# Performance work log

Hardware: AMD Instinct MI355X
Metric: run time of the kernel (lower is better)

The kernel has to match this reference:

```python
import jax, jax.numpy as jnp
import numpy as np

N_NODES = 100000
N_EDGES = 1600000
IN_DIM = 64
EMBED_DIM = 128
OUT_DIM = 10


def setup_inputs() -> dict:
    key = jax.random.key(0)
    ks = jax.random.split(key, 12)
    x = jax.random.normal(ks[0], (N_NODES, IN_DIM), dtype=jnp.float32)
    edge_index = jax.random.randint(ks[1], (2, N_EDGES), 0, N_NODES, dtype=jnp.int64)
    s = lambda k, shp, fan_in: jax.random.normal(k, shp, dtype=jnp.float32) / np.sqrt(fan_in)
    # SAGEConv params: lin_l (applied to aggregated neighbors, has bias), lin_r (root, no bias)
    W_l = s(ks[2], (IN_DIM, EMBED_DIM), IN_DIM)
    b_l = jnp.zeros((EMBED_DIM,), dtype=jnp.float32)
    W_r = s(ks[3], (IN_DIM, EMBED_DIM), IN_DIM)
    # Classifier MLP: embed -> 64 -> 128 -> out
    W1 = s(ks[4], (EMBED_DIM, 64), EMBED_DIM)
    b1 = jnp.zeros((64,), dtype=jnp.float32)
    W2 = s(ks[5], (64, 128), 64)
    b2 = jnp.zeros((128,), dtype=jnp.float32)
    W3 = s(ks[6], (128, OUT_DIM), 128)
    b3 = jnp.zeros((OUT_DIM,), dtype=jnp.float32)
    return {"x": x, "edge_index": edge_index, "W_l": W_l, "b_l": b_l, "W_r": W_r,
            "W1": W1, "b1": b1, "W2": W2, "b2": b2, "W3": W3, "b3": b3}


def reference(x, edge_index, W_l, b_l, W_r, W1, b1, W2, b2, W3, b3):
    src, dst = edge_index[0], edge_index[1]
    # mean-aggregate neighbor features: gather x[src], scatter-sum to dst, divide by degree
    msg = x[src]                                                   # [E, in_dim]
    agg = jax.ops.segment_sum(msg, dst, num_segments=N_NODES)      # [N, in_dim]
    deg = jax.ops.segment_sum(jnp.ones((src.shape[0],), x.dtype), dst, num_segments=N_NODES)
    mean = agg / jnp.maximum(deg, 1.0)[:, None]                    # [N, in_dim]
    # SAGEConv: lin_l(mean_neigh) + lin_r(x_root)
    h = mean @ W_l + b_l + x @ W_r                                 # [N, embed_dim]
    # classifier MLP (logits)
    h = jax.nn.relu(h @ W1 + b1)
    h = jax.nn.relu(h @ W2 + b2)
    return h @ W3 + b3
```

## Files before the change

### kernel.cpp

```cpp
#include <hip/hip_runtime.h>
#include <hip/hip_bf16.h>

#define N_NODES 100000
#define IN_DIM 64
#define EMB 128
#define HID1 64
#define HID2 128
#define OUT_DIM 10

#define CHUNK 4096
#define EPT   (CHUNK / 256)
#define NBUCK ((N_NODES + 511) >> 9)
#define CAPB 9216

#define NB_CONV ((N_NODES * 16) / 256)
#define WCAT_N (128 * 128)
#define W1T_N  (64 * 128)
#define W2T_N  (128 * 64)
#define W3T_N  (16 * 128)
#define PREP_TOT (WCAT_N + W1T_N + W2T_N + W3T_N)
#define NB_PREP ((PREP_TOT + 255) / 256)

using short8 = __attribute__((ext_vector_type(8))) short;
using bfx4   = __attribute__((ext_vector_type(4))) short;
using f32x4  = __attribute__((ext_vector_type(4))) float;

__device__ inline short f2bf(float f) {
  __hip_bfloat16 h = __float2bfloat16(f);
  return *reinterpret_cast<short*>(&h);
}

struct BinShared {
  int hist[NBUCK], excl[NBUCK], cur[NBUCK], gb[NBUCK];
  int stage[CHUNK];
  unsigned char bof[CHUNK];
  int sc[256];
};

__global__ __launch_bounds__(256) void frontend_kernel(
    const float* __restrict__ x,
    const int* __restrict__ src, const int* __restrict__ dst,
    const float* __restrict__ W_l, const float* __restrict__ W_r,
    const float* __restrict__ W1, const float* __restrict__ W2,
    const float* __restrict__ W3,
    int* __restrict__ gcur, int* __restrict__ ebuf, short* __restrict__ comb,
    short* __restrict__ wcat_t, short* __restrict__ w1t,
    short* __restrict__ w2t, short* __restrict__ w3t,
    int E, int nbC)
{
  __shared__ __align__(16) char smem_raw[sizeof(BinShared)];
  const int b = blockIdx.x;
  const int tid = threadIdx.x;

  if (b < nbC) {
    BinShared& S = *reinterpret_cast<BinShared*>(smem_raw);
    const int base = b * CHUNK;
    const int cn = min(CHUNK, E - base);

    int dreg[EPT];
#pragma unroll
    for (int it = 0; it < EPT; ++it) {
      int i = tid + it * 256;
      dreg[it] = (i < cn) ? dst[base + i] : -1;
    }

    for (int i = tid; i < NBUCK; i += 256) S.hist[i] = 0;
    __syncthreads();
#pragma unroll
    for (int it = 0; it < EPT; ++it)
      if (dreg[it] >= 0) atomicAdd(&S.hist[dreg[it] >> 9], 1);
    __syncthreads();

    int v = (tid < NBUCK) ? S.hist[tid] : 0;
    S.sc[tid] = v;
    __syncthreads();
    for (int off = 1; off < 256; off <<= 1) {
      int u = (tid >= off) ? S.sc[tid - off] : 0;
      __syncthreads();
      S.sc[tid] += u;
      __syncthreads();
    }
    if (tid < NBUCK) {
      int ex = S.sc[tid] - v;
      S.excl[tid] = ex; S.cur[tid] = ex;
      S.gb[tid] = v ? atomicAdd(&gcur[tid], v) : 0;
    }
    __syncthreads();

#pragma unroll
    for (int it = 0; it < EPT; ++it) {
      int i = tid + it * 256;
      if (i < cn) {
        int d = dreg[it], s = src[base + i];
        int bk = d >> 9;
        int pos = atomicAdd(&S.cur[bk], 1);
        S.stage[pos] = ((d & 511) << 17) | s;
        S.bof[pos] = (unsigned char)bk;
      }
    }
    __syncthreads();

    for (int i = tid; i < cn; i += 256) {
      int bk = S.bof[i];
      int idx = S.gb[bk] + (i - S.excl[bk]);
      if (idx < CAPB) ebuf[bk * CAPB + idx] = S.stage[i];
    }
  } else if (b < nbC + NB_CONV) {
    int t = (b - nbC) * 256 + tid;
    int node = t >> 4, g = t & 15;
    f32x4 v = *(const f32x4*)&x[(size_t)node * IN_DIM + g * 4];
    bfx4 s;
#pragma unroll
    for (int i = 0; i < 4; ++i) s[i] = f2bf(v[i]);
    *(bfx4*)&comb[((size_t)node << 7) + g * 4] = s;
  } else {
    int t = (b - nbC - NB_CONV) * 256 + tid;
    if (t < WCAT_N) {
      int c = t >> 7, k = t & 127;
      float v = (k < 64) ? W_r[k * EMB + c] : W_l[(k - 64) * EMB + c];
      wcat_t[c * 128 + k] = f2bf(v);
    } else if (t < WCAT_N + W1T_N) {
      int u = t - WCAT_N;
      int c = u >> 7, k = u & 127;
      w1t[c * 128 + k] = f2bf(W1[k * HID1 + c]);
    } else if (t < WCAT_N + W1T_N + W2T_N) {
      int u = t - WCAT_N - W1T_N;
      int c = u >> 6, k = u & 63;
      w2t[c * 64 + k] = f2bf(W2[k * HID2 + c]);
    } else if (t < PREP_TOT) {
      int u = t - WCAT_N - W1T_N - W2T_N;
      int c = u >> 7, k = u & 127;
      w3t[c * 128 + k] = (c < OUT_DIM) ? f2bf(W3[k * OUT_DIM + c]) : (short)0;
    }
  }
}

__global__ __launch_bounds__(256) void bucket_csr(
    const int* __restrict__ gcur, int* __restrict__ ebuf,
    int* __restrict__ offs, int* __restrict__ oend)
{
  __shared__ int cnt[512], cur[512], sc[512];
  __shared__ int ep[CAPB];
  __shared__ int es[CAPB];
  const int b = blockIdx.x, tid = threadIdx.x;
  const int node0 = b << 9;
  const int nn = min(512, N_NODES - node0);
  const int ebase = b * CAPB;
  const int ecnt = min(gcur[b], CAPB);

  for (int i = tid; i < 512; i += 256) cnt[i] = 0;
  __syncthreads();
  for (int i = tid; i < ecnt; i += 256) {
    int p = ebuf[ebase + i];
    ep[i] = p;
    atomicAdd(&cnt[p >> 17], 1);
  }
  __syncthreads();
  for (int i = tid; i < 512; i += 256) sc[i] = cnt[i];
  __syncthreads();
  for (int off = 1; off < 512; off <<= 1) {
    int i0 = tid, i1 = tid + 256;
    int v0 = (i0 >= off) ? sc[i0 - off] : 0;
    int v1 = (i1 >= off) ? sc[i1 - off] : 0;
    __syncthreads();
    sc[i0] += v0; sc[i1] += v1;
    __syncthreads();
  }
  for (int i = tid; i < 512; i += 256) {
    int ex = sc[i] - cnt[i];
    cur[i] = ex;
    if (i < nn) {
      offs[node0 + i] = ebase + ex;
      oend[node0 + i] = ebase + sc[i];
    }
  }
  __syncthreads();
  for (int i = tid; i < ecnt; i += 256) {
    int p = ep[i];
    int pos = atomicAdd(&cur[p >> 17], 1);
    es[pos] = p & 131071;
  }
  __syncthreads();
  for (int i = tid; i < ecnt; i += 256) ebuf[ebase + i] = es[i];
}

__global__ __launch_bounds__(256) void aggregate_kernel(
    const int* __restrict__ offs, const int* __restrict__ oend,
    const int* __restrict__ esrc, short* __restrict__ comb)
{
  int wv = (int)((blockIdx.x * 256 + threadIdx.x) >> 6);
  const int lane = threadIdx.x & 63;
  const int node = __builtin_amdgcn_readfirstlane(wv);
  if (node >= N_NODES) return;
  const int beg = offs[node];
  const int end = oend[node];
  const int deg = end - beg;
  const unsigned short* cb = (const unsigned short*)comb;
  float a = 0.f;

  int k = beg;
  for (; k + 16 <= end; k += 16) {
    unsigned o0  = ((unsigned)esrc[k]      << 7) + lane;
    unsigned o1  = ((unsigned)esrc[k + 1]  << 7) + lane;
    unsigned o2  = ((unsigned)esrc[k + 2]  << 7) + lane;
    unsigned o3  = ((unsigned)esrc[k + 3]  << 7) + lane;
    unsigned o4  = ((unsigned)esrc[k + 4]  << 7) + lane;
    unsigned o5  = ((unsigned)esrc[k + 5]  << 7) + lane;
    unsigned o6  = ((unsigned)esrc[k + 6]  << 7) + lane;
    unsigned o7  = ((unsigned)esrc[k + 7]  << 7) + lane;
    unsigned o8  = ((unsigned)esrc[k + 8]  << 7) + lane;
    unsigned o9  = ((unsigned)esrc[k + 9]  << 7) + lane;
    unsigned o10 = ((unsigned)esrc[k + 10] << 7) + lane;
    unsigned o11 = ((unsigned)esrc[k + 11] << 7) + lane;
    unsigned o12 = ((unsigned)esrc[k + 12] << 7) + lane;
    unsigned o13 = ((unsigned)esrc[k + 13] << 7) + lane;
    unsigned o14 = ((unsigned)esrc[k + 14] << 7) + lane;
    unsigned o15 = ((unsigned)esrc[k + 15] << 7) + lane;
    unsigned u0  = cb[o0],  u1  = cb[o1],  u2  = cb[o2],  u3  = cb[o3];
    unsigned u4  = cb[o4],  u5  = cb[o5],  u6  = cb[o6],  u7  = cb[o7];
    unsigned u8  = cb[o8],  u9  = cb[o9],  u10 = cb[o10], u11 = cb[o11];
    unsigned u12 = cb[o12], u13 = cb[o13], u14 = cb[o14], u15 = cb[o15];
    a += __uint_as_float(u0  << 16); a += __uint_as_float(u1  << 16);
    a += __uint_as_float(u2  << 16); a += __uint_as_float(u3  << 16);
    a += __uint_as_float(u4  << 16); a += __uint_as_float(u5  << 16);
    a += __uint_as_float(u6  << 16); a += __uint_as_float(u7  << 16);
    a += __uint_as_float(u8  << 16); a += __uint_as_float(u9  << 16);
    a += __uint_as_float(u10 << 16); a += __uint_as_float(u11 << 16);
    a += __uint_as_float(u12 << 16); a += __uint_as_float(u13 << 16);
    a += __uint_as_float(u14 << 16); a += __uint_as_float(u15 << 16);
  }
  if (k + 8 <= end) {
    unsigned o0 = ((unsigned)esrc[k]     << 7) + lane;
    unsigned o1 = ((unsigned)esrc[k + 1] << 7) + lane;
    unsigned o2 = ((unsigned)esrc[k + 2] << 7) + lane;
    unsigned o3 = ((unsigned)esrc[k + 3] << 7) + lane;
    unsigned o4 = ((unsigned)esrc[k + 4] << 7) + lane;
    unsigned o5 = ((unsigned)esrc[k + 5] << 7) + lane;
    unsigned o6 = ((unsigned)esrc[k + 6] << 7) + lane;
    unsigned o7 = ((unsigned)esrc[k + 7] << 7) + lane;
    unsigned u0 = cb[o0], u1 = cb[o1], u2 = cb[o2], u3 = cb[o3];
    unsigned u4 = cb[o4], u5 = cb[o5], u6 = cb[o6], u7 = cb[o7];
    a += __uint_as_float(u0 << 16); a += __uint_as_float(u1 << 16);
    a += __uint_as_float(u2 << 16); a += __uint_as_float(u3 << 16);
    a += __uint_as_float(u4 << 16); a += __uint_as_float(u5 << 16);
    a += __uint_as_float(u6 << 16); a += __uint_as_float(u7 << 16);
    k += 8;
  }
  if (k + 4 <= end) {
    unsigned o0 = ((unsigned)esrc[k]     << 7) + lane;
    unsigned o1 = ((unsigned)esrc[k + 1] << 7) + lane;
    unsigned o2 = ((unsigned)esrc[k + 2] << 7) + lane;
    unsigned o3 = ((unsigned)esrc[k + 3] << 7) + lane;
    unsigned u0 = cb[o0], u1 = cb[o1], u2 = cb[o2], u3 = cb[o3];
    a += __uint_as_float(u0 << 16); a += __uint_as_float(u1 << 16);
    a += __uint_as_float(u2 << 16); a += __uint_as_float(u3 << 16);
    k += 4;
  }
  for (; k < end; ++k) {
    unsigned u0 = cb[((unsigned)esrc[k] << 7) + lane];
    a += __uint_as_float(u0 << 16);
  }

  float m = a / fmaxf((float)deg, 1.0f);
  ((unsigned short*)comb)[((size_t)node << 7) + 64 + lane] =
      (unsigned short)f2bf(m);
}

#define PA 128
#define PH 64

__global__ __launch_bounds__(256) void fused_mfma_kernel(
    const short* __restrict__ comb,
    const short* __restrict__ wcat_t, const short* __restrict__ w1t,
    const short* __restrict__ w2t, const short* __restrict__ w3t,
    const float* __restrict__ b_l, const float* __restrict__ b1,
    const float* __restrict__ b2, const float* __restrict__ b3,
    float* __restrict__ out)
{
  __shared__ __align__(16) short sA0[64 * PA];
  __shared__ __align__(16) short sH [64 * PA];
  __shared__ __align__(16) short sH1[64 * PH];
  __shared__ __align__(16) short sW [128 * PA];

  const int tid  = threadIdx.x;
  const int base = blockIdx.x * 64;
  const int lane = tid & 63;
  const int w    = tid >> 6;
  const int lrow = lane & 15;
  const int lgrp = lane >> 4;

  for (int T = tid; T < 1024; T += 256) {
    int n = T >> 4, g = T & 15;
    int node = base + n;
    short8 s = {0, 0, 0, 0, 0, 0, 0, 0};
    if (node < N_NODES) s = *(const short8*)&comb[(size_t)node * 128 + 8 * g];
    *(short8*)&sA0[(n * PA + 8 * g) ^ ((n & 7) << 3)] = s;
  }
  for (int T = tid; T < 2048; T += 256) {
    int c = T >> 4, kg = T & 15;
    *(short8*)&sW[(c * PA + 8 * kg) ^ ((c & 7) << 3)] =
        *(const short8*)&wcat_t[c * 128 + 8 * kg];
  }
  __syncthreads();

  {
    const int c0w = 32 * w;
    short8 bf[2][4];
#pragma unroll
    for (int ct = 0; ct < 2; ++ct)
#pragma unroll
      for (int kk = 0; kk < 4; ++kk) {
        int row = c0w + 16 * ct + lrow;
        bf[ct][kk] = *(const short8*)&sW[(row * PA + kk * 32 + lgrp * 8) ^ ((row & 7) << 3)];
      }
#pragma unroll
    for (int rt = 0; rt < 4; ++rt) {
      short8 af[4];
#pragma unroll
      for (int kk = 0; kk < 4; ++kk) {
        int row = rt * 16 + lrow;
        af[kk] = *(const short8*)&sA0[(row * PA + kk * 32 + lgrp * 8) ^ ((row & 7) << 3)];
      }
#pragma unroll
      for (int ct = 0; ct < 2; ++ct) {
        float bv = b_l[c0w + 16 * ct + lrow];
        f32x4 acc = {bv, bv, bv, bv};
#pragma unroll
        for (int kk = 0; kk < 4; ++kk)
          acc = __builtin_amdgcn_mfma_f32_16x16x32_bf16(af[kk], bf[ct][kk], acc, 0, 0, 0);
        int col = c0w + 16 * ct + lrow;
        int rb = rt * 16 + lgrp * 4;
#pragma unroll
        for (int r = 0; r < 4; ++r) {
          int row = rb + r;
          sH[(row * PA + col) ^ ((row & 7) << 3)] = f2bf(acc[r]);
        }
      }
    }
  }
  __syncthreads();

  for (int T = tid; T < 1024; T += 256) {
    int c = T >> 4, kg = T & 15;
    *(short8*)&sW[(c * PA + 8 * kg) ^ ((c & 7) << 3)] =
        *(const short8*)&w1t[c * 128 + 8 * kg];
  }
  {
    int c = tid >> 4, kg = tid & 15;
    *(short8*)&sA0[(c * PA + 8 * kg) ^ ((c & 7) << 3)] =
        *(const short8*)&w3t[c * 128 + 8 * kg];
  }
  __syncthreads();

  {
    const int c0 = 16 * w;
    short8 bf[4];
#pragma unroll
    for (int kk = 0; kk < 4; ++kk) {
      int row = c0 + lrow;
      bf[kk] = *(const short8*)&sW[(row * PA + kk * 32 + lgrp * 8) ^ ((row & 7) << 3)];
    }
#pragma unroll
    for (int rt = 0; rt < 4; ++rt) {
      short8 af[4];
#pragma unroll
      for (int kk = 0; kk < 4; ++kk) {
        int row = rt * 16 + lrow;
        af[kk] = *(const short8*)&sH[(row * PA + kk * 32 + lgrp * 8) ^ ((row & 7) << 3)];
      }
      float bv = b1[c0 + lrow];
      f32x4 acc = {bv, bv, bv, bv};
#pragma unroll
      for (int kk = 0; kk < 4; ++kk)
        acc = __builtin_amdgcn_mfma_f32_16x16x32_bf16(af[kk], bf[kk], acc, 0, 0, 0);
      int col = c0 + lrow;
      int rb = rt * 16 + lgrp * 4;
#pragma unroll
      for (int r = 0; r < 4; ++r) {
        int row = rb + r;
        sH1[(row * PH + col) ^ ((row & 7) << 3)] = f2bf(fmaxf(acc[r], 0.f));
      }
    }
  }
  __syncthreads();

  for (int T = tid; T < 1024; T += 256) {
    int c = T >> 3, kg = T & 7;
    *(short8*)&sW[(c * PA + 8 * kg) ^ ((c & 7) << 3)] =
        *(const short8*)&w2t[c * 64 + 8 * kg];
  }
  __syncthreads();

  {
    const int c0w = 32 * w;
    short8 bf[2][2];
#pragma unroll
    for (int ct = 0; ct < 2; ++ct)
#pragma unroll
      for (int kk = 0; kk < 2; ++kk) {
        int row = c0w + 16 * ct + lrow;
        bf[ct][kk] = *(const short8*)&sW[(row * PA + kk * 32 + lgrp * 8) ^ ((row & 7) << 3)];
      }
#pragma unroll
    for (int rt = 0; rt < 4; ++rt) {
      short8 af[2];
#pragma unroll
      for (int kk = 0; kk < 2; ++kk) {
        int row = rt * 16 + lrow;
        af[kk] = *(const short8*)&sH1[(row * PH + kk * 32 + lgrp * 8) ^ ((row & 7) << 3)];
      }
#pragma unroll
      for (int ct = 0; ct < 2; ++ct) {
        float bv = b2[c0w + 16 * ct + lrow];
        f32x4 acc = {bv, bv, bv, bv};
#pragma unroll
        for (int kk = 0; kk < 2; ++kk)
          acc = __builtin_amdgcn_mfma_f32_16x16x32_bf16(af[kk], bf[ct][kk], acc, 0, 0, 0);
        int col = c0w + 16 * ct + lrow;
        int rb = rt * 16 + lgrp * 4;
#pragma unroll
        for (int r = 0; r < 4; ++r) {
          int row = rb + r;
          sH[(row * PA + col) ^ ((row & 7) << 3)] = f2bf(fmaxf(acc[r], 0.f));
        }
      }
    }
  }
  __syncthreads();

  {
    short8 af[4], bf[4];
#pragma unroll
    for (int kk = 0; kk < 4; ++kk) {
      int row = 16 * w + lrow;
      af[kk] = *(const short8*)&sH[(row * PA + kk * 32 + lgrp * 8) ^ ((row & 7) << 3)];
      bf[kk] = *(const short8*)&sA0[(lrow * PA + kk * 32 + lgrp * 8) ^ ((lrow & 7) << 3)];
    }
    float bv = (lrow < OUT_DIM) ? b3[lrow] : 0.f;
    f32x4 acc = {bv, bv, bv, bv};
#pragma unroll
    for (int kk = 0; kk < 4; ++kk)
      acc = __builtin_amdgcn_mfma_f32_16x16x32_bf16(af[kk], bf[kk], acc, 0, 0, 0);
#pragma unroll
    for (int r = 0; r < 4; ++r) {
      int row = 16 * w + lgrp * 4 + r;
      int node = base + row;
      if (node < N_NODES && lrow < OUT_DIM)
        out[(long long)node * OUT_DIM + lrow] = acc[r];
    }
  }
}

extern "C" void kernel_launch(void* const* d_in, const int* in_sizes, int n_in,
                              void* d_out, int out_size, void* d_ws, size_t ws_size,
                              hipStream_t stream) {
  const float* x   = (const float*)d_in[0];
  const int*   ei  = (const int*)d_in[1];
  const float* W_l = (const float*)d_in[2];
  const float* b_l = (const float*)d_in[3];
  const float* W_r = (const float*)d_in[4];
  const float* W1  = (const float*)d_in[5];
  const float* b1  = (const float*)d_in[6];
  const float* W2  = (const float*)d_in[7];
  const float* b2  = (const float*)d_in[8];
  const float* W3  = (const float*)d_in[9];
  const float* b3  = (const float*)d_in[10];
  float* out = (float*)d_out;

  const int E = in_sizes[1] / 2;
  const int* src = ei;
  const int* dst = ei + E;

  short* wcat_t = (short*)d_ws;
  short* w1t    = wcat_t + WCAT_N;
  short* w2t    = w1t + W1T_N;
  short* w3t    = w2t + W2T_N;
  short* comb   = w3t + W3T_N;
  int*   offs   = (int*)(comb + (size_t)N_NODES * 128);
  int*   oend   = offs + N_NODES;
  int*   ebuf   = oend + N_NODES;
  int*   gcur   = ebuf + (size_t)NBUCK * CAPB;

  (void)hipMemsetAsync(gcur, 0, NBUCK * sizeof(int), stream);

  const int nbC = (E + CHUNK - 1) / CHUNK;
  frontend_kernel<<<nbC + NB_CONV + NB_PREP, 256, 0, stream>>>(
      x, src, dst, W_l, W_r, W1, W2, W3,
      gcur, ebuf, comb, wcat_t, w1t, w2t, w3t, E, nbC);

  bucket_csr<<<NBUCK, 256, 0, stream>>>(gcur, ebuf, offs, oend);

  int nbAgg = (N_NODES * 64 + 255) / 256;
  aggregate_kernel<<<nbAgg, 256, 0, stream>>>(offs, oend, ebuf, comb);

  int nbF = (N_NODES + 63) / 64;
  fused_mfma_kernel<<<nbF, 256, 0, stream>>>(comb, wcat_t, w1t, w2t, w3t,
                                             b_l, b1, b2, b3, out);
}
```

Before: 109.5 us.

## Double fused MLP tile to 128 nodes with 512-thread blocks

The fused MFMA kernel now handles 128 nodes per block with 8 waves instead of 64 nodes with 4 waves. The work split is rearranged so each wave owns one 16-column slice across all rows, and the second layer splits rows across two wave groups. This amortises the per-block staging of weights into LDS over more nodes, but raises LDS use per block, which may limit how many blocks fit on a CU and how well barriers overlap. The binning shared arrays are also padded to 256 entries so the scan write-back loses its thread guard.

```diff
diff --git a/kernel.cpp b/kernel.cpp
--- a/kernel.cpp
+++ b/kernel.cpp
@@ -31,7 +31,7 @@
 }
 
 struct BinShared {
-  int hist[NBUCK], excl[NBUCK], cur[NBUCK], gb[NBUCK];
+  int hist[256], excl[256], cur[256], gb[256];
   int stage[CHUNK];
   unsigned char bof[CHUNK];
   int sc[256];
@@ -64,7 +64,7 @@
       dreg[it] = (i < cn) ? dst[base + i] : -1;
     }
 
-    for (int i = tid; i < NBUCK; i += 256) S.hist[i] = 0;
+    for (int i = tid; i < 256; i += 256) S.hist[i] = 0;
     __syncthreads();
 #pragma unroll
     for (int it = 0; it < EPT; ++it)
@@ -80,10 +80,10 @@
       S.sc[tid] += u;
       __syncthreads();
     }
-    if (tid < NBUCK) {
+    {
       int ex = S.sc[tid] - v;
       S.excl[tid] = ex; S.cur[tid] = ex;
-      S.gb[tid] = v ? atomicAdd(&gcur[tid], v) : 0;
+      S.gb[tid] = (tid < NBUCK && v) ? atomicAdd(&gcur[tid], v) : 0;
     }
     __syncthreads();
 
@@ -269,7 +269,7 @@
 #define PA 128
 #define PH 64
 
-__global__ __launch_bounds__(256) void fused_mfma_kernel(
+__global__ __launch_bounds__(512) void fused_mfma_kernel(
     const short* __restrict__ comb,
     const short* __restrict__ wcat_t, const short* __restrict__ w1t,
     const short* __restrict__ w2t, const short* __restrict__ w3t,
@@ -277,26 +277,26 @@
     const float* __restrict__ b2, const float* __restrict__ b3,
     float* __restrict__ out)
 {
-  __shared__ __align__(16) short sA0[64 * PA];
-  __shared__ __align__(16) short sH [64 * PA];
-  __shared__ __align__(16) short sH1[64 * PH];
+  __shared__ __align__(16) short sA0[128 * PA];
+  __shared__ __align__(16) short sH [128 * PA];
+  __shared__ __align__(16) short sH1[128 * PH];
   __shared__ __align__(16) short sW [128 * PA];
 
   const int tid  = threadIdx.x;
-  const int base = blockIdx.x * 64;
+  const int base = blockIdx.x * 128;
   const int lane = tid & 63;
   const int w    = tid >> 6;
   const int lrow = lane & 15;
   const int lgrp = lane >> 4;
 
-  for (int T = tid; T < 1024; T += 256) {
+  for (int T = tid; T < 2048; T += 512) {
     int n = T >> 4, g = T & 15;
     int node = base + n;
     short8 s = {0, 0, 0, 0, 0, 0, 0, 0};
     if (node < N_NODES) s = *(const short8*)&comb[(size_t)node * 128 + 8 * g];
     *(short8*)&sA0[(n * PA + 8 * g) ^ ((n & 7) << 3)] = s;
   }
-  for (int T = tid; T < 2048; T += 256) {
+  for (int T = tid; T < 2048; T += 512) {
     int c = T >> 4, kg = T & 15;
     *(short8*)&sW[(c * PA + 8 * kg) ^ ((c & 7) << 3)] =
         *(const short8*)&wcat_t[c * 128 + 8 * kg];
@@ -304,71 +304,22 @@
   __syncthreads();
 
   {
-    const int c0w = 32 * w;
-    short8 bf[2][4];
-#pragma unroll
-    for (int ct = 0; ct < 2; ++ct)
-#pragma unroll
-      for (int kk = 0; kk < 4; ++kk) {
-        int row = c0w + 16 * ct + lrow;
-        bf[ct][kk] = *(const short8*)&sW[(row * PA + kk * 32 + lgrp * 8) ^ ((row & 7) << 3)];
-      }
-#pragma unroll
-    for (int rt = 0; rt < 4; ++rt) {
+    const int c0 = 16 * w;
+    short8 bf[4];
+#pragma unroll
+    for (int kk = 0; kk < 4; ++kk) {
+      int row = c0 + lrow;
+      bf[kk] = *(const short8*)&sW[(row * PA + kk * 32 + lgrp * 8) ^ ((row & 7) << 3)];
+    }
+#pragma unroll
+    for (int rt = 0; rt < 8; ++rt) {
       short8 af[4];
 #pragma unroll
       for (int kk = 0; kk < 4; ++kk) {
         int row = rt * 16 + lrow;
         af[kk] = *(const short8*)&sA0[(row * PA + kk * 32 + lgrp * 8) ^ ((row & 7) << 3)];
       }
-#pragma unroll
-      for (int ct = 0; ct < 2; ++ct) {
-        float bv = b_l[c0w + 16 * ct + lrow];
-        f32x4 acc = {bv, bv, bv, bv};
-#pragma unroll
-        for (int kk = 0; kk < 4; ++kk)
-          acc = __builtin_amdgcn_mfma_f32_16x16x32_bf16(af[kk], bf[ct][kk], acc, 0, 0, 0);
-        int col = c0w + 16 * ct + lrow;
-        int rb = rt * 16 + lgrp * 4;
-#pragma unroll
-        for (int r = 0; r < 4; ++r) {
-          int row = rb + r;
-          sH[(row * PA + col) ^ ((row & 7) << 3)] = f2bf(acc[r]);
-        }
-      }
-    }
-  }
-  __syncthreads();
-
-  for (int T = tid; T < 1024; T += 256) {
-    int c = T >> 4, kg = T & 15;
-    *(short8*)&sW[(c * PA + 8 * kg) ^ ((c & 7) << 3)] =
-        *(const short8*)&w1t[c * 128 + 8 * kg];
-  }
-  {
-    int c = tid >> 4, kg = tid & 15;
-    *(short8*)&sA0[(c * PA + 8 * kg) ^ ((c & 7) << 3)] =
-        *(const short8*)&w3t[c * 128 + 8 * kg];
-  }
-  __syncthreads();
-
-  {
-    const int c0 = 16 * w;
-    short8 bf[4];
-#pragma unroll
-    for (int kk = 0; kk < 4; ++kk) {
-      int row = c0 + lrow;
-      bf[kk] = *(const short8*)&sW[(row * PA + kk * 32 + lgrp * 8) ^ ((row & 7) << 3)];
-    }
-#pragma unroll
-    for (int rt = 0; rt < 4; ++rt) {
-      short8 af[4];
-#pragma unroll
-      for (int kk = 0; kk < 4; ++kk) {
-        int row = rt * 16 + lrow;
-        af[kk] = *(const short8*)&sH[(row * PA + kk * 32 + lgrp * 8) ^ ((row & 7) << 3)];
-      }
-      float bv = b1[c0 + lrow];
+      float bv = b_l[c0 + lrow];
       f32x4 acc = {bv, bv, bv, bv};
 #pragma unroll
       for (int kk = 0; kk < 4; ++kk)
@@ -378,13 +329,58 @@
 #pragma unroll
       for (int r = 0; r < 4; ++r) {
         int row = rb + r;
+        sH[(row * PA + col) ^ ((row & 7) << 3)] = f2bf(acc[r]);
+      }
+    }
+  }
+  __syncthreads();
+
+  for (int T = tid; T < 1024; T += 512) {
+    int c = T >> 4, kg = T & 15;
+    *(short8*)&sW[(c * PA + 8 * kg) ^ ((c & 7) << 3)] =
+        *(const short8*)&w1t[c * 128 + 8 * kg];
+  }
+  if (tid < 256) {
+    int c = tid >> 4, kg = tid & 15;
+    *(short8*)&sA0[(c * PA + 8 * kg) ^ ((c & 7) << 3)] =
+        *(const short8*)&w3t[c * 128 + 8 * kg];
+  }
+  __syncthreads();
+
+  {
+    const int c0 = 16 * (w & 3);
+    const int r0 = 64 * (w >> 2);
+    short8 bf[4];
+#pragma unroll
+    for (int kk = 0; kk < 4; ++kk) {
+      int row = c0 + lrow;
+      bf[kk] = *(const short8*)&sW[(row * PA + kk * 32 + lgrp * 8) ^ ((row & 7) << 3)];
+    }
+#pragma unroll
+    for (int rt = 0; rt < 4; ++rt) {
+      short8 af[4];
+#pragma unroll
+      for (int kk = 0; kk < 4; ++kk) {
+        int row = r0 + rt * 16 + lrow;
+        af[kk] = *(const short8*)&sH[(row * PA + kk * 32 + lgrp * 8) ^ ((row & 7) << 3)];
+      }
+      float bv = b1[c0 + lrow];
+      f32x4 acc = {bv, bv, bv, bv};
+#pragma unroll
+      for (int kk = 0; kk < 4; ++kk)
+        acc = __builtin_amdgcn_mfma_f32_16x16x32_bf16(af[kk], bf[kk], acc, 0, 0, 0);
+      int col = c0 + lrow;
+      int rb = r0 + rt * 16 + lgrp * 4;
+#pragma unroll
+      for (int r = 0; r < 4; ++r) {
+        int row = rb + r;
         sH1[(row * PH + col) ^ ((row & 7) << 3)] = f2bf(fmaxf(acc[r], 0.f));
       }
     }
   }
   __syncthreads();
 
-  for (int T = tid; T < 1024; T += 256) {
+  for (int T = tid; T < 1024; T += 512) {
     int c = T >> 3, kg = T & 7;
     *(short8*)&sW[(c * PA + 8 * kg) ^ ((c & 7) << 3)] =
         *(const short8*)&w2t[c * 64 + 8 * kg];
@@ -392,37 +388,32 @@
   __syncthreads();
 
   {
-    const int c0w = 32 * w;
-    short8 bf[2][2];
-#pragma unroll
-    for (int ct = 0; ct < 2; ++ct)
-#pragma unroll
-      for (int kk = 0; kk < 2; ++kk) {
-        int row = c0w + 16 * ct + lrow;
-        bf[ct][kk] = *(const short8*)&sW[(row * PA + kk * 32 + lgrp * 8) ^ ((row & 7) << 3)];
-      }
-#pragma unroll
-    for (int rt = 0; rt < 4; ++rt) {
+    const int c0 = 16 * w;
+    short8 bf[2];
+#pragma unroll
+    for (int kk = 0; kk < 2; ++kk) {
+      int row = c0 + lrow;
+      bf[kk] = *(const short8*)&sW[(row * PA + kk * 32 + lgrp * 8) ^ ((row & 7) << 3)];
+    }
+#pragma unroll
+    for (int rt = 0; rt < 8; ++rt) {
       short8 af[2];
 #pragma unroll
       for (int kk = 0; kk < 2; ++kk) {
         int row = rt * 16 + lrow;
         af[kk] = *(const short8*)&sH1[(row * PH + kk * 32 + lgrp * 8) ^ ((row & 7) << 3)];
       }
-#pragma unroll
-      for (int ct = 0; ct < 2; ++ct) {
-        float bv = b2[c0w + 16 * ct + lrow];
-        f32x4 acc = {bv, bv, bv, bv};
-#pragma unroll
-        for (int kk = 0; kk < 2; ++kk)
-          acc = __builtin_amdgcn_mfma_f32_16x16x32_bf16(af[kk], bf[ct][kk], acc, 0, 0, 0);
-        int col = c0w + 16 * ct + lrow;
-        int rb = rt * 16 + lgrp * 4;
-#pragma unroll
-        for (int r = 0; r < 4; ++r) {
-          int row = rb + r;
-          sH[(row * PA + col) ^ ((row & 7) << 3)] = f2bf(fmaxf(acc[r], 0.f));
-        }
+      float bv = b2[c0 + lrow];
+      f32x4 acc = {bv, bv, bv, bv};
+#pragma unroll
+      for (int kk = 0; kk < 2; ++kk)
+        acc = __builtin_amdgcn_mfma_f32_16x16x32_bf16(af[kk], bf[kk], acc, 0, 0, 0);
+      int col = c0 + lrow;
+      int rb = rt * 16 + lgrp * 4;
+#pragma unroll
+      for (int r = 0; r < 4; ++r) {
+        int row = rb + r;
+        sH[(row * PA + col) ^ ((row & 7) << 3)] = f2bf(fmaxf(acc[r], 0.f));
       }
     }
   }
@@ -493,7 +484,7 @@
   int nbAgg = (N_NODES * 64 + 255) / 256;
   aggregate_kernel<<<nbAgg, 256, 0, stream>>>(offs, oend, ebuf, comb);
 
-  int nbF = (N_NODES + 63) / 64;
-  fused_mfma_kernel<<<nbF, 256, 0, stream>>>(comb, wcat_t, w1t, w2t, w3t,
+  int nbF = (N_NODES + 127) / 128;
+  fused_mfma_kernel<<<nbF, 512, 0, stream>>>(comb, wcat_t, w1t, w2t, w3t,
                                              b_l, b1, b2, b3, out);
 }
```

Measured after the change: 112.5 us. +2.7%, slower.
